# Kernel tuning notes

Hardware: AMD Instinct MI355X
Metric: run time of the kernel (lower is better)

Reference implementation:

```python
import jax, jax.numpy as jnp
import numpy as np

N = 50000      # nodes
E = 800000     # message edges
P = 200000     # prediction edges
C_IN = 64      # in_channels
C_H = 64       # hidden_channels


def setup_inputs() -> dict:
    key = jax.random.key(0)
    ks = jax.random.split(key, 20)
    s = 0.05
    inp = {
        "x": jax.random.normal(ks[0], (N, C_IN), jnp.float32),
        "prediction_edges": jax.random.randint(ks[1], (2, P), 0, N, dtype=jnp.int32),
        "message_edges": jax.random.randint(ks[2], (2, E), 0, N, dtype=jnp.int32),
        "message_edgewt": jax.random.uniform(ks[3], (E,), jnp.float32),
        # conv1 params
        "coef1": jnp.float32(0.5),
        "pool1_w": jax.random.normal(ks[4], (C_IN, C_IN), jnp.float32) * s,
        "pool1_b": jnp.zeros((C_IN,), jnp.float32),
        "fin1_w": jax.random.normal(ks[5], (C_H, 2 * C_IN), jnp.float32) * s,
        "fin1_b": jnp.zeros((C_H,), jnp.float32),
        # conv2 params
        "coef2": jnp.float32(0.5),
        "pool2_w": jax.random.normal(ks[6], (C_H, C_H), jnp.float32) * s,
        "pool2_b": jnp.zeros((C_H,), jnp.float32),
        "fin2_w": jax.random.normal(ks[7], (C_H, 2 * C_H), jnp.float32) * s,
        "fin2_b": jnp.zeros((C_H,), jnp.float32),
        # edge heads
        "ewp_w": jax.random.normal(ks[8], (1, 2 * C_H), jnp.float32) * s,
        "ewp_b": jnp.zeros((1,), jnp.float32),
        "ep_w": jax.random.normal(ks[9], (1, 2 * C_H), jnp.float32) * s,
        "ep_b": jnp.zeros((1,), jnp.float32),
    }
    return inp


def _relu(v):
    return jnp.maximum(v, 0)


def _sage_conv(x, src, dst, ew, coef, pw, pb, fw, fb):
    n = x.shape[0]
    all_src = jnp.concatenate([src, dst])   # [2E]
    all_dst = jnp.concatenate([dst, src])   # [2E]
    neigh = x[all_src]                       # [2E, C] gather
    w2 = jnp.concatenate([ew, ew])           # [2E]
    edge_feat = neigh * (1.0 + coef * w2[:, None])
    pooled = _relu(edge_feat @ pw.T + pb)    # [2E, C]
    # self-loop edges (src == dst) routed to dummy segment n
    seg = jnp.where(all_src != all_dst, all_dst, n)
    agg = jax.ops.segment_max(pooled, seg, num_segments=n + 1)[:n]
    agg = jnp.where(jnp.isfinite(agg), agg, 0.0)  # empty nodes -> 0
    h = jnp.concatenate([x, agg], axis=-1)   # [N, 2C]
    return _relu(h @ fw.T + fb)


def reference(x, prediction_edges, message_edges, message_edgewt,
              coef1, pool1_w, pool1_b, fin1_w, fin1_b,
              coef2, pool2_w, pool2_b, fin2_w, fin2_b,
              ewp_w, ewp_b, ep_w, ep_b):
    src, dst = message_edges[0], message_edges[1]
    h = _sage_conv(x, src, dst, message_edgewt, coef1, pool1_w, pool1_b, fin1_w, fin1_b)
    h = _sage_conv(h, src, dst, message_edgewt, coef2, pool2_w, pool2_b, fin2_w, fin2_b)
    emb = jnp.concatenate([h[prediction_edges[0]], h[prediction_edges[1]]], axis=-1)  # [P, 2C]
    edge_weights = _relu(emb @ ewp_w.T + ewp_b)   # [P, 1]
    edge_predictor = emb @ ep_w.T + ep_b          # [P, 1]
    return edge_weights, edge_predictor
```

## Files before the change

kernel.cpp:

```cpp
#include <hip/hip_runtime.h>


typedef _Float16 h16;
typedef __attribute__((ext_vector_type(4))) _Float16 h16x4;
typedef __attribute__((ext_vector_type(4))) float f32x4;
#define MFMA16(a, b, c) __builtin_amdgcn_mfma_f32_16x16x16f16(a, b, c, 0, 0, 0)

#define NBMAX 1600
#define NFB   128

__global__ void hist_kernel(const int* __restrict__ esrc,
                            const int* __restrict__ edst,
                            int* __restrict__ bucketTotal,
                            int* __restrict__ blockBase, int E, int NB) {
    __shared__ int cnt[NBMAX];
    for (int b = threadIdx.x; b < NB; b += blockDim.x) cnt[b] = 0;
    __syncthreads();
    const int chunk = (E + gridDim.x - 1) / gridDim.x;
    const int start = blockIdx.x * chunk;
    const int end = min(start + chunk, E);
    for (int e = start + (int)threadIdx.x; e < end; e += blockDim.x) {
        const int s = esrc[e];
        const int d = edst[e];
        if (s != d) {
            atomicAdd(&cnt[d >> 5], 1);
            atomicAdd(&cnt[s >> 5], 1);
        }
    }
    __syncthreads();
    for (int b = threadIdx.x; b < NB; b += blockDim.x)
        blockBase[(size_t)blockIdx.x * NB + b] = atomicAdd(&bucketTotal[b], cnt[b]);
}

__global__ void scan_kernel(const int* __restrict__ deg,
                            int* __restrict__ offs, int n) {
    __shared__ int wsum[16];
    __shared__ int s_carry;
    const int tid = threadIdx.x;
    const int lane = tid & 63;
    const int wid = tid >> 6;
    if (tid == 0) s_carry = 0;
    __syncthreads();
    for (int base = 0; base < n; base += 1024) {
        const int i = base + tid;
        const int v = (i < n) ? deg[i] : 0;
        int x = v;
#pragma unroll
        for (int off = 1; off < 64; off <<= 1) {
            int t = __shfl_up(x, off, 64);
            if (lane >= off) x += t;
        }
        if (lane == 63) wsum[wid] = x;
        __syncthreads();
        if (wid == 0) {
            int wv = (lane < 16) ? wsum[lane] : 0;
#pragma unroll
            for (int off = 1; off < 16; off <<= 1) {
                int t = __shfl_up(wv, off, 64);
                if (lane >= off) wv += t;
            }
            if (lane < 16) wsum[lane] = wv;
        }
        __syncthreads();
        const int carry = s_carry;
        const int waveoff = (wid > 0) ? wsum[wid - 1] : 0;
        if (i < n) offs[i] = carry + waveoff + x - v;
        __syncthreads();
        if (tid == 0) s_carry = carry + wsum[15];
        __syncthreads();
    }
}

__global__ void binfill_kernel(const int* __restrict__ esrc,
                               const int* __restrict__ edst,
                               const float* __restrict__ ewt,
                               const int* __restrict__ bucketStart,
                               const int* __restrict__ blockBase,
                               unsigned* __restrict__ entries, int E, int NB) {
    __shared__ int cur[NBMAX];
    for (int b = threadIdx.x; b < NB; b += blockDim.x)
        cur[b] = bucketStart[b] + blockBase[(size_t)blockIdx.x * NB + b];
    __syncthreads();
    const int chunk = (E + gridDim.x - 1) / gridDim.x;
    const int start = blockIdx.x * chunk;
    const int end = min(start + chunk, E);
    for (int e = start + (int)threadIdx.x; e < end; e += blockDim.x) {
        const int s = esrc[e];
        const int d = edst[e];
        if (s != d) {
            const unsigned wq =
                (unsigned)fminf(ewt[e] * 2048.f + 0.5f, 2047.f) << 21;
            const int pd = atomicAdd(&cur[d >> 5], 1);
            entries[pd] = (unsigned)s | ((unsigned)(d & 31) << 16) | wq;
            const int ps = atomicAdd(&cur[s >> 5], 1);
            entries[ps] = (unsigned)d | ((unsigned)(s & 31) << 16) | wq;
        }
    }
}

__global__ void sortbucket_kernel(const int* __restrict__ bucketStart,
                                  const int* __restrict__ bucketTotal,
                                  const unsigned* __restrict__ in,
                                  unsigned* __restrict__ out,
                                  int* __restrict__ nodeBeg, int n, int NB) {
    __shared__ int bin[32];
    __shared__ int cur[32];
    const int bkt = blockIdx.x;
    const int beg = bucketStart[bkt];
    const int cnt = bucketTotal[bkt];
    if (threadIdx.x < 32) bin[threadIdx.x] = 0;
    __syncthreads();
    for (int i = threadIdx.x; i < cnt; i += blockDim.x)
        atomicAdd(&bin[(in[beg + i] >> 16) & 31u], 1);
    __syncthreads();
    if (threadIdx.x == 0) {
        int run = 0;
#pragma unroll
        for (int r = 0; r < 32; ++r) { cur[r] = run; run += bin[r]; }
    }
    __syncthreads();
    if (threadIdx.x < 32) {
        const int node = bkt * 32 + (int)threadIdx.x;
        if (node < n) nodeBeg[node] = beg + cur[threadIdx.x];
    }
    if (bkt == NB - 1 && threadIdx.x == 0) nodeBeg[n] = beg + cnt;
    __syncthreads();
    for (int i = threadIdx.x; i < cnt; i += blockDim.x) {
        const unsigned e = in[beg + i];
        const int pos = beg + atomicAdd(&cur[(e >> 16) & 31u], 1);
        out[pos] = e;
    }
}

template <bool XFP32>
__global__ __launch_bounds__(256, 2)
void mmA_kernel(const void* __restrict__ Xv, const float* __restrict__ W,
                h16* __restrict__ Z, int ntiles) {
    const int lane = threadIdx.x & 63;
    const int c = lane & 15, q = lane >> 4;
    int wave = (int)((blockIdx.x * blockDim.x + threadIdx.x) >> 6);
    const int nwaves = (int)((gridDim.x * blockDim.x) >> 6);
    h16x4 bf[4][4];
#pragma unroll
    for (int ct = 0; ct < 4; ++ct)
#pragma unroll
        for (int ks = 0; ks < 4; ++ks) {
            const float4 w4 = *(const float4*)(W + (ct * 16 + c) * 64 + ks * 16 + q * 4);
            bf[ct][ks] = (h16x4){(h16)w4.x, (h16)w4.y, (h16)w4.z, (h16)w4.w};
        }
    for (int t = wave; t < ntiles; t += nwaves) {
        const int n0 = t * 16;
        h16x4 af[4];
        if constexpr (XFP32) {
            const float* xr = (const float*)Xv + (size_t)(n0 + c) * 64 + q * 4;
#pragma unroll
            for (int ks = 0; ks < 4; ++ks) {
                const float4 v = *(const float4*)(xr + ks * 16);
                af[ks] = (h16x4){(h16)v.x, (h16)v.y, (h16)v.z, (h16)v.w};
            }
        } else {
            const h16* xr = (const h16*)Xv + (size_t)(n0 + c) * 64 + q * 4;
#pragma unroll
            for (int ks = 0; ks < 4; ++ks) af[ks] = *(const h16x4*)(xr + ks * 16);
        }
        f32x4 acc[4];
#pragma unroll
        for (int ct = 0; ct < 4; ++ct) acc[ct] = (f32x4){0.f, 0.f, 0.f, 0.f};
#pragma unroll
        for (int ct = 0; ct < 4; ++ct)
#pragma unroll
            for (int ks = 0; ks < 4; ++ks)
                acc[ct] = MFMA16(af[ks], bf[ct][ks], acc[ct]);
#pragma unroll
        for (int ct = 0; ct < 4; ++ct)
#pragma unroll
            for (int m = 0; m < 4; ++m)
                Z[(size_t)(n0 + q * 4 + m) * 64 + ct * 16 + c] = (h16)acc[ct][m];
    }
}

__global__ void aggregateN_kernel(const int* __restrict__ nodeBeg,
                                  const unsigned* __restrict__ entries,
                                  const h16* __restrict__ Z,
                                  const float* __restrict__ pb,
                                  const float* __restrict__ coefp,
                                  h16* __restrict__ agg, int n) {
    const int lane = threadIdx.x & 63;
    int wave = (int)((blockIdx.x * blockDim.x + threadIdx.x) >> 6);
    const int nwaves = (int)((gridDim.x * blockDim.x) >> 6);
    const float coefq = coefp[0] * (1.f / 2048.f);
    const float pbc = pb[lane];
    for (int d = wave; d < n; d += nwaves) {
        const int du = __builtin_amdgcn_readfirstlane(d);
        const int beg = nodeBeg[du];
        const int end = nodeBeg[du + 1];
        float m0 = 0.f, m1 = 0.f, m2 = 0.f, m3 = 0.f;
        int i = beg;
        for (; i + 4 <= end; i += 4) {
            const unsigned e0 = (unsigned)__builtin_amdgcn_readfirstlane((int)entries[i]);
            const unsigned e1 = (unsigned)__builtin_amdgcn_readfirstlane((int)entries[i + 1]);
            const unsigned e2 = (unsigned)__builtin_amdgcn_readfirstlane((int)entries[i + 2]);
            const unsigned e3 = (unsigned)__builtin_amdgcn_readfirstlane((int)entries[i + 3]);
            const float z0 = (float)Z[(size_t)(e0 & 0xffffu) * 64 + lane];
            const float z1 = (float)Z[(size_t)(e1 & 0xffffu) * 64 + lane];
            const float z2 = (float)Z[(size_t)(e2 & 0xffffu) * 64 + lane];
            const float z3 = (float)Z[(size_t)(e3 & 0xffffu) * 64 + lane];
            m0 = fmaxf(m0, fmaf(fmaf(coefq, (float)(e0 >> 21), 1.f), z0, pbc));
            m1 = fmaxf(m1, fmaf(fmaf(coefq, (float)(e1 >> 21), 1.f), z1, pbc));
            m2 = fmaxf(m2, fmaf(fmaf(coefq, (float)(e2 >> 21), 1.f), z2, pbc));
            m3 = fmaxf(m3, fmaf(fmaf(coefq, (float)(e3 >> 21), 1.f), z3, pbc));
        }
        for (; i < end; ++i) {
            const unsigned e = (unsigned)__builtin_amdgcn_readfirstlane((int)entries[i]);
            const float zv = (float)Z[(size_t)(e & 0xffffu) * 64 + lane];
            m0 = fmaxf(m0, fmaf(fmaf(coefq, (float)(e >> 21), 1.f), zv, pbc));
        }
        agg[(size_t)du * 64 + lane] = (h16)fmaxf(fmaxf(m0, m1), fmaxf(m2, m3));
    }
}

template <bool XFP32>
__global__ __launch_bounds__(256, 2)
void finA_kernel(const void* __restrict__ XA, const h16* __restrict__ XB,
                 const float* __restrict__ W, const float* __restrict__ b,
                 h16* __restrict__ H, int ntiles) {
    const int lane = threadIdx.x & 63;
    const int c = lane & 15, q = lane >> 4;
    int wave = (int)((blockIdx.x * blockDim.x + threadIdx.x) >> 6);
    const int nwaves = (int)((gridDim.x * blockDim.x) >> 6);
    h16x4 bf[4][8];
#pragma unroll
    for (int ct = 0; ct < 4; ++ct)
#pragma unroll
        for (int ks = 0; ks < 8; ++ks) {
            const float4 w4 = *(const float4*)(W + (ct * 16 + c) * 128 + ks * 16 + q * 4);
            bf[ct][ks] = (h16x4){(h16)w4.x, (h16)w4.y, (h16)w4.z, (h16)w4.w};
        }
    float bc[4];
#pragma unroll
    for (int ct = 0; ct < 4; ++ct) bc[ct] = b[ct * 16 + c];
    for (int t = wave; t < ntiles; t += nwaves) {
        const int n0 = t * 16;
        h16x4 af[8];
        if constexpr (XFP32) {
            const float* ra = (const float*)XA + (size_t)(n0 + c) * 64 + q * 4;
#pragma unroll
            for (int ks = 0; ks < 4; ++ks) {
                const float4 v = *(const float4*)(ra + ks * 16);
                af[ks] = (h16x4){(h16)v.x, (h16)v.y, (h16)v.z, (h16)v.w};
            }
        } else {
            const h16* ra = (const h16*)XA + (size_t)(n0 + c) * 64 + q * 4;
#pragma unroll
            for (int ks = 0; ks < 4; ++ks) af[ks] = *(const h16x4*)(ra + ks * 16);
        }
        const h16* rb = XB + (size_t)(n0 + c) * 64 + q * 4;
#pragma unroll
        for (int ks = 0; ks < 4; ++ks) af[4 + ks] = *(const h16x4*)(rb + ks * 16);
        f32x4 acc[4];
#pragma unroll
        for (int ct = 0; ct < 4; ++ct) acc[ct] = (f32x4){bc[ct], bc[ct], bc[ct], bc[ct]};
#pragma unroll
        for (int ct = 0; ct < 4; ++ct)
#pragma unroll
            for (int ks = 0; ks < 8; ++ks)
                acc[ct] = MFMA16(af[ks], bf[ct][ks], acc[ct]);
#pragma unroll
        for (int ct = 0; ct < 4; ++ct)
#pragma unroll
            for (int m = 0; m < 4; ++m)
                H[(size_t)(n0 + q * 4 + m) * 64 + ct * 16 + c] =
                    (h16)fmaxf(acc[ct][m], 0.f);
    }
}

__global__ __launch_bounds__(256, 2)
void fin2A_kernel(const h16* __restrict__ XA, const h16* __restrict__ XB,
                  const float* __restrict__ W, const float* __restrict__ b,
                  const float* __restrict__ ewp_w, const float* __restrict__ ep_w,
                  float4* __restrict__ nodeheads, int ntiles) {
    const int lane = threadIdx.x & 63;
    const int c = lane & 15, q = lane >> 4;
    int wave = (int)((blockIdx.x * blockDim.x + threadIdx.x) >> 6);
    const int nwaves = (int)((gridDim.x * blockDim.x) >> 6);
    h16x4 bf[4][8];
#pragma unroll
    for (int ct = 0; ct < 4; ++ct)
#pragma unroll
        for (int ks = 0; ks < 8; ++ks) {
            const float4 w4 = *(const float4*)(W + (ct * 16 + c) * 128 + ks * 16 + q * 4);
            bf[ct][ks] = (h16x4){(h16)w4.x, (h16)w4.y, (h16)w4.z, (h16)w4.w};
        }
    float bc[4], hw1s[4], hw1d[4], hw2s[4], hw2d[4];
#pragma unroll
    for (int ct = 0; ct < 4; ++ct) {
        bc[ct] = b[ct * 16 + c];
        hw1s[ct] = ewp_w[ct * 16 + c];
        hw1d[ct] = ewp_w[64 + ct * 16 + c];
        hw2s[ct] = ep_w[ct * 16 + c];
        hw2d[ct] = ep_w[64 + ct * 16 + c];
    }
    for (int t = wave; t < ntiles; t += nwaves) {
        const int n0 = t * 16;
        const h16* __restrict__ ra = XA + (size_t)(n0 + c) * 64 + q * 4;
        const h16* __restrict__ rb = XB + (size_t)(n0 + c) * 64 + q * 4;
        h16x4 af[8];
#pragma unroll
        for (int ks = 0; ks < 4; ++ks) {
            af[ks] = *(const h16x4*)(ra + ks * 16);
            af[4 + ks] = *(const h16x4*)(rb + ks * 16);
        }
        f32x4 acc[4];
#pragma unroll
        for (int ct = 0; ct < 4; ++ct) acc[ct] = (f32x4){bc[ct], bc[ct], bc[ct], bc[ct]};
#pragma unroll
        for (int ct = 0; ct < 4; ++ct)
#pragma unroll
            for (int ks = 0; ks < 8; ++ks)
                acc[ct] = MFMA16(af[ks], bf[ct][ks], acc[ct]);
        f32x4 r1 = {0.f, 0.f, 0.f, 0.f}, r2 = r1, r3 = r1, r4 = r1;
#pragma unroll
        for (int ct = 0; ct < 4; ++ct)
#pragma unroll
            for (int m = 0; m < 4; ++m) {
                const float h = fmaxf(acc[ct][m], 0.f);
                r1[m] = fmaf(hw1s[ct], h, r1[m]);
                r2[m] = fmaf(hw1d[ct], h, r2[m]);
                r3[m] = fmaf(hw2s[ct], h, r3[m]);
                r4[m] = fmaf(hw2d[ct], h, r4[m]);
            }
#pragma unroll
        for (int off = 1; off < 16; off <<= 1)
#pragma unroll
            for (int m = 0; m < 4; ++m) {
                r1[m] += __shfl_xor(r1[m], off, 16);
                r2[m] += __shfl_xor(r2[m], off, 16);
                r3[m] += __shfl_xor(r3[m], off, 16);
                r4[m] += __shfl_xor(r4[m], off, 16);
            }
        if (c == 0) {
#pragma unroll
            for (int m = 0; m < 4; ++m)
                nodeheads[n0 + q * 4 + m] =
                    make_float4(r1[m], r2[m], r3[m], r4[m]);
        }
    }
}

__global__ void headsP_kernel(const int* __restrict__ psrc,
                              const int* __restrict__ pdst,
                              const float4* __restrict__ nodeheads,
                              const float* __restrict__ ewp_b,
                              const float* __restrict__ ep_b,
                              float* __restrict__ out, int P) {
    int t = blockIdx.x * blockDim.x + threadIdx.x;
    const int stride = gridDim.x * blockDim.x;
    const float b1 = ewp_b[0], b2 = ep_b[0];
    for (; t < P; t += stride) {
        const float4 qs = nodeheads[psrc[t]];
        const float4 qd = nodeheads[pdst[t]];
        out[t] = fmaxf(qs.x + qd.y + b1, 0.f);
        out[(size_t)P + t] = qs.z + qd.w + b2;
    }
}

extern "C" void kernel_launch(void* const* d_in, const int* in_sizes, int n_in,
                              void* d_out, int out_size, void* d_ws, size_t ws_size,
                              hipStream_t stream) {
    const float* x      = (const float*)d_in[0];
    const int*   pe     = (const int*)d_in[1];
    const int*   me     = (const int*)d_in[2];
    const float* mew    = (const float*)d_in[3];
    const float* coef1  = (const float*)d_in[4];
    const float* p1w    = (const float*)d_in[5];
    const float* p1b    = (const float*)d_in[6];
    const float* f1w    = (const float*)d_in[7];
    const float* f1b    = (const float*)d_in[8];
    const float* coef2  = (const float*)d_in[9];
    const float* p2w    = (const float*)d_in[10];
    const float* p2b    = (const float*)d_in[11];
    const float* f2w    = (const float*)d_in[12];
    const float* f2b    = (const float*)d_in[13];
    const float* ewp_w  = (const float*)d_in[14];
    const float* ewp_b  = (const float*)d_in[15];
    const float* ep_w   = (const float*)d_in[16];
    const float* ep_b   = (const float*)d_in[17];

    const int n = in_sizes[0] / 64;
    const int P = in_sizes[1] / 2;
    const int E = in_sizes[2] / 2;
    const int NB = (n + 31) >> 5;
    const int ntiles = (n + 15) >> 4;

    float4* nodeheads = (float4*)d_ws;
    h16* z16   = (h16*)(nodeheads + n);
    h16* agg16 = z16 + (size_t)n * 64;
    h16* h1    = agg16 + (size_t)n * 64;
    unsigned* entriesA = (unsigned*)(h1 + (size_t)n * 64);
    unsigned* entriesB = entriesA + 2 * (size_t)E;
    int* bucketTotal = (int*)(entriesB + 2 * (size_t)E);
    int* bucketStart = bucketTotal + NBMAX;
    int* nodeBeg     = bucketStart + NBMAX;
    int* blockBase   = nodeBeg + (n + 1);

    const int* esrc = me;
    const int* edst = me + E;
    const int* psrc = pe;
    const int* pdst = pe + P;

    const dim3 blk(256);
    const int mfGrid = (ntiles + 3) / 4;
    const int agGrid = 2048;
    const int hpGrid = (P + 255) / 256;

    hipMemsetAsync(bucketTotal, 0, (size_t)NB * sizeof(int), stream);
    hist_kernel<<<NFB, blk, 0, stream>>>(esrc, edst, bucketTotal, blockBase, E, NB);
    scan_kernel<<<1, 1024, 0, stream>>>(bucketTotal, bucketStart, NB);
    binfill_kernel<<<NFB, blk, 0, stream>>>(esrc, edst, mew, bucketStart,
                                            blockBase, entriesA, E, NB);
    sortbucket_kernel<<<NB, blk, 0, stream>>>(bucketStart, bucketTotal,
                                              entriesA, entriesB, nodeBeg, n, NB);

    mmA_kernel<true><<<mfGrid, blk, 0, stream>>>(x, p1w, z16, ntiles);
    aggregateN_kernel<<<agGrid, blk, 0, stream>>>(nodeBeg, entriesB, z16,
                                                  p1b, coef1, agg16, n);
    finA_kernel<true><<<mfGrid, blk, 0, stream>>>(x, agg16, f1w, f1b, h1, ntiles);

    mmA_kernel<false><<<mfGrid, blk, 0, stream>>>(h1, p2w, z16, ntiles);
    aggregateN_kernel<<<agGrid, blk, 0, stream>>>(nodeBeg, entriesB, z16,
                                                  p2b, coef2, agg16, n);
    fin2A_kernel<<<mfGrid, blk, 0, stream>>>(h1, agg16, f2w, f2b,
                                             ewp_w, ep_w, nodeheads, ntiles);

    headsP_kernel<<<hpGrid, blk, 0, stream>>>(psrc, pdst, nodeheads,
                                              ewp_b, ep_b, (float*)d_out, P);
}
```

Baseline: 201.3 us.

## Fuse bucket scan into binfill, fuse fin1 with pool2 matmul, pair-node aggregation

The separate single-block scan kernel is removed: every binfill block now recomputes the bucket prefix sum in LDS, and block 0 writes bucketStart for the later sort. The layer-1 final linear kernel now also applies the pool2 matmul through an LDS transpose, so the separate mmA launch and its re-read of h1 go away. The aggregation kernel handles two destination nodes per wave with interleaved edge loops, giving more independent gathers in flight per wave. The cost is redundant scan work in every binfill block and higher register and LDS use in the fused kernels.

New measurement: 191.0 us. 1.05x faster.

```diff
diff --git a/kernel.cpp b/kernel.cpp
--- a/kernel.cpp
+++ b/kernel.cpp
@@ -32,67 +32,54 @@
         blockBase[(size_t)blockIdx.x * NB + b] = atomicAdd(&bucketTotal[b], cnt[b]);
 }
 
-__global__ void scan_kernel(const int* __restrict__ deg,
-                            int* __restrict__ offs, int n) {
-    __shared__ int wsum[16];
-    __shared__ int s_carry;
+__global__ void binfill_kernel(const int* __restrict__ esrc,
+                               const int* __restrict__ edst,
+                               const float* __restrict__ ewt,
+                               const int* __restrict__ bucketTotal,
+                               int* __restrict__ bucketStart,
+                               const int* __restrict__ blockBase,
+                               unsigned* __restrict__ entries, int E, int NB) {
+    __shared__ int sv[NBMAX];
+    __shared__ int wls[4];
     const int tid = threadIdx.x;
     const int lane = tid & 63;
     const int wid = tid >> 6;
-    if (tid == 0) s_carry = 0;
-    __syncthreads();
-    for (int base = 0; base < n; base += 1024) {
-        const int i = base + tid;
-        const int v = (i < n) ? deg[i] : 0;
-        int x = v;
-#pragma unroll
-        for (int off = 1; off < 64; off <<= 1) {
-            int t = __shfl_up(x, off, 64);
-            if (lane >= off) x += t;
-        }
-        if (lane == 63) wsum[wid] = x;
-        __syncthreads();
-        if (wid == 0) {
-            int wv = (lane < 16) ? wsum[lane] : 0;
-#pragma unroll
-            for (int off = 1; off < 16; off <<= 1) {
-                int t = __shfl_up(wv, off, 64);
-                if (lane >= off) wv += t;
-            }
-            if (lane < 16) wsum[lane] = wv;
-        }
-        __syncthreads();
-        const int carry = s_carry;
-        const int waveoff = (wid > 0) ? wsum[wid - 1] : 0;
-        if (i < n) offs[i] = carry + waveoff + x - v;
-        __syncthreads();
-        if (tid == 0) s_carry = carry + wsum[15];
-        __syncthreads();
-    }
-}
-
-__global__ void binfill_kernel(const int* __restrict__ esrc,
-                               const int* __restrict__ edst,
-                               const float* __restrict__ ewt,
-                               const int* __restrict__ bucketStart,
-                               const int* __restrict__ blockBase,
-                               unsigned* __restrict__ entries, int E, int NB) {
-    __shared__ int cur[NBMAX];
-    for (int b = threadIdx.x; b < NB; b += blockDim.x)
-        cur[b] = bucketStart[b] + blockBase[(size_t)blockIdx.x * NB + b];
+    for (int b = tid; b < NB; b += blockDim.x) sv[b] = bucketTotal[b];
+    __syncthreads();
+    const int CH = (NB + 255) / 256;
+    const int lo = tid * CH, hi = min(lo + CH, NB);
+    int sum = 0;
+    for (int i = lo; i < hi; ++i) sum += sv[i];
+    int x = sum;
+#pragma unroll
+    for (int off = 1; off < 64; off <<= 1) {
+        int t = __shfl_up(x, off, 64);
+        if (lane >= off) x += t;
+    }
+    if (lane == 63) wls[wid] = x;
+    __syncthreads();
+    int wof = 0;
+    for (int w = 0; w < wid; ++w) wof += wls[w];
+    int run = wof + x - sum;
+    for (int i = lo; i < hi; ++i) { const int v = sv[i]; sv[i] = run; run += v; }
+    __syncthreads();
+    if (blockIdx.x == 0)
+        for (int b = tid; b < NB; b += blockDim.x) bucketStart[b] = sv[b];
+    for (int b = tid; b < NB; b += blockDim.x)
+        sv[b] += blockBase[(size_t)blockIdx.x * NB + b];
     __syncthreads();
     const int chunk = (E + gridDim.x - 1) / gridDim.x;
     const int start = blockIdx.x * chunk;
     const int end = min(start + chunk, E);
-    for (int e = start + (int)threadIdx.x; e < end; e += blockDim.x) {
+    for (int e = start + (int)tid; e < end; e += blockDim.x) {
         const int s = esrc[e];
         const int d = edst[e];
         if (s != d) {
             const unsigned wq =
                 (unsigned)fminf(ewt[e] * 2048.f + 0.5f, 2047.f) << 21;
-            const int pd = atomicAdd(&cur[d >> 5], 1);
+            const int pd = atomicAdd(&sv[d >> 5], 1);
             entries[pd] = (unsigned)s | ((unsigned)(d & 31) << 16) | wq;
-            const int ps = atomicAdd(&cur[s >> 5], 1);
+            const int ps = atomicAdd(&sv[s >> 5], 1);
             entries[ps] = (unsigned)d | ((unsigned)(s & 31) << 16) | wq;
         }
     }
@@ -179,7 +166,13 @@
     }
 }
 
-__global__ void aggregateN_kernel(const int* __restrict__ nodeBeg,
+#define EDGE_STEP(eV, mV)                                                      \
+    {                                                                          \
+        const float zv = (float)Z[(size_t)((eV) & 0xffffu) * 64 + lane];       \
+        mV = fmaxf(mV, fmaf(fmaf(coefq, (float)((eV) >> 21), 1.f), zv, pbc));  \
+    }
+
+__global__ void aggregateP_kernel(const int* __restrict__ nodeBeg,
                                   const unsigned* __restrict__ entries,
                                   const h16* __restrict__ Z,
                                   const float* __restrict__ pb,
@@ -190,69 +183,96 @@
     const int nwaves = (int)((gridDim.x * blockDim.x) >> 6);
     const float coefq = coefp[0] * (1.f / 2048.f);
     const float pbc = pb[lane];
-    for (int d = wave; d < n; d += nwaves) {
-        const int du = __builtin_amdgcn_readfirstlane(d);
-        const int beg = nodeBeg[du];
-        const int end = nodeBeg[du + 1];
-        float m0 = 0.f, m1 = 0.f, m2 = 0.f, m3 = 0.f;
-        int i = beg;
-        for (; i + 4 <= end; i += 4) {
-            const unsigned e0 = (unsigned)__builtin_amdgcn_readfirstlane((int)entries[i]);
-            const unsigned e1 = (unsigned)__builtin_amdgcn_readfirstlane((int)entries[i + 1]);
-            const unsigned e2 = (unsigned)__builtin_amdgcn_readfirstlane((int)entries[i + 2]);
-            const unsigned e3 = (unsigned)__builtin_amdgcn_readfirstlane((int)entries[i + 3]);
-            const float z0 = (float)Z[(size_t)(e0 & 0xffffu) * 64 + lane];
-            const float z1 = (float)Z[(size_t)(e1 & 0xffffu) * 64 + lane];
-            const float z2 = (float)Z[(size_t)(e2 & 0xffffu) * 64 + lane];
-            const float z3 = (float)Z[(size_t)(e3 & 0xffffu) * 64 + lane];
-            m0 = fmaxf(m0, fmaf(fmaf(coefq, (float)(e0 >> 21), 1.f), z0, pbc));
-            m1 = fmaxf(m1, fmaf(fmaf(coefq, (float)(e1 >> 21), 1.f), z1, pbc));
-            m2 = fmaxf(m2, fmaf(fmaf(coefq, (float)(e2 >> 21), 1.f), z2, pbc));
-            m3 = fmaxf(m3, fmaf(fmaf(coefq, (float)(e3 >> 21), 1.f), z3, pbc));
-        }
-        for (; i < end; ++i) {
-            const unsigned e = (unsigned)__builtin_amdgcn_readfirstlane((int)entries[i]);
-            const float zv = (float)Z[(size_t)(e & 0xffffu) * 64 + lane];
-            m0 = fmaxf(m0, fmaf(fmaf(coefq, (float)(e >> 21), 1.f), zv, pbc));
-        }
-        agg[(size_t)du * 64 + lane] = (h16)fmaxf(fmaxf(m0, m1), fmaxf(m2, m3));
-    }
-}
-
-template <bool XFP32>
+    const int npairs = (n + 1) >> 1;
+    for (int p = wave; p < npairs; p += nwaves) {
+        const int dA = __builtin_amdgcn_readfirstlane(2 * p);
+        const int dB = dA + 1;
+        const int begA = nodeBeg[dA];
+        const int endA = nodeBeg[dA + 1];
+        int iB = endA, endB = endA;
+        if (dB < n) endB = nodeBeg[dB + 1];
+        float mA0 = 0.f, mA1 = 0.f, mA2 = 0.f, mA3 = 0.f;
+        float mB0 = 0.f, mB1 = 0.f, mB2 = 0.f, mB3 = 0.f;
+        int iA = begA;
+        while (iA + 4 <= endA && iB + 4 <= endB) {
+            const unsigned a0 = (unsigned)__builtin_amdgcn_readfirstlane((int)entries[iA]);
+            const unsigned a1 = (unsigned)__builtin_amdgcn_readfirstlane((int)entries[iA + 1]);
+            const unsigned a2 = (unsigned)__builtin_amdgcn_readfirstlane((int)entries[iA + 2]);
+            const unsigned a3 = (unsigned)__builtin_amdgcn_readfirstlane((int)entries[iA + 3]);
+            const unsigned b0 = (unsigned)__builtin_amdgcn_readfirstlane((int)entries[iB]);
+            const unsigned b1 = (unsigned)__builtin_amdgcn_readfirstlane((int)entries[iB + 1]);
+            const unsigned b2 = (unsigned)__builtin_amdgcn_readfirstlane((int)entries[iB + 2]);
+            const unsigned b3 = (unsigned)__builtin_amdgcn_readfirstlane((int)entries[iB + 3]);
+            EDGE_STEP(a0, mA0) EDGE_STEP(a1, mA1) EDGE_STEP(a2, mA2) EDGE_STEP(a3, mA3)
+            EDGE_STEP(b0, mB0) EDGE_STEP(b1, mB1) EDGE_STEP(b2, mB2) EDGE_STEP(b3, mB3)
+            iA += 4; iB += 4;
+        }
+        for (; iA + 4 <= endA; iA += 4) {
+            const unsigned a0 = (unsigned)__builtin_amdgcn_readfirstlane((int)entries[iA]);
+            const unsigned a1 = (unsigned)__builtin_amdgcn_readfirstlane((int)entries[iA + 1]);
+            const unsigned a2 = (unsigned)__builtin_amdgcn_readfirstlane((int)entries[iA + 2]);
+            const unsigned a3 = (unsigned)__builtin_amdgcn_readfirstlane((int)entries[iA + 3]);
+            EDGE_STEP(a0, mA0) EDGE_STEP(a1, mA1) EDGE_STEP(a2, mA2) EDGE_STEP(a3, mA3)
+        }
+        for (; iB + 4 <= endB; iB += 4) {
+            const unsigned b0 = (unsigned)__builtin_amdgcn_readfirstlane((int)entries[iB]);
+            const unsigned b1 = (unsigned)__builtin_amdgcn_readfirstlane((int)entries[iB + 1]);
+            const unsigned b2 = (unsigned)__builtin_amdgcn_readfirstlane((int)entries[iB + 2]);
+            const unsigned b3 = (unsigned)__builtin_amdgcn_readfirstlane((int)entries[iB + 3]);
+            EDGE_STEP(b0, mB0) EDGE_STEP(b1, mB1) EDGE_STEP(b2, mB2) EDGE_STEP(b3, mB3)
+        }
+        for (; iA < endA; ++iA) {
+            const unsigned a0 = (unsigned)__builtin_amdgcn_readfirstlane((int)entries[iA]);
+            EDGE_STEP(a0, mA0)
+        }
+        for (; iB < endB; ++iB) {
+            const unsigned b0 = (unsigned)__builtin_amdgcn_readfirstlane((int)entries[iB]);
+            EDGE_STEP(b0, mB0)
+        }
+        agg[(size_t)dA * 64 + lane] = (h16)fmaxf(fmaxf(mA0, mA1), fmaxf(mA2, mA3));
+        if (dB < n)
+            agg[(size_t)dB * 64 + lane] = (h16)fmaxf(fmaxf(mB0, mB1), fmaxf(mB2, mB3));
+    }
+}
+
 __global__ __launch_bounds__(256, 2)
-void finA_kernel(const void* __restrict__ XA, const h16* __restrict__ XB,
-                 const float* __restrict__ W, const float* __restrict__ b,
-                 h16* __restrict__ H, int ntiles) {
+void finAmm_kernel(const float* __restrict__ XA, const h16* __restrict__ XB,
+                   const float* __restrict__ W, const float* __restrict__ b,
+                   const float* __restrict__ W2,
+                   h16* __restrict__ H, h16* __restrict__ Z2, int ntiles) {
+    __shared__ h16 ldsT[4][16 * 68];
     const int lane = threadIdx.x & 63;
+    const int wid = threadIdx.x >> 6;
     const int c = lane & 15, q = lane >> 4;
     int wave = (int)((blockIdx.x * blockDim.x + threadIdx.x) >> 6);
     const int nwaves = (int)((gridDim.x * blockDim.x) >> 6);
-    h16x4 bf[4][8];
-#pragma unroll
-    for (int ct = 0; ct < 4; ++ct)
+    h16x4 bf[4][8], bf2[4][4];
+#pragma unroll
+    for (int ct = 0; ct < 4; ++ct) {
 #pragma unroll
         for (int ks = 0; ks < 8; ++ks) {
             const float4 w4 = *(const float4*)(W + (ct * 16 + c) * 128 + ks * 16 + q * 4);
             bf[ct][ks] = (h16x4){(h16)w4.x, (h16)w4.y, (h16)w4.z, (h16)w4.w};
         }
+#pragma unroll
+        for (int ks = 0; ks < 4; ++ks) {
+            const float4 w4 = *(const float4*)(W2 + (ct * 16 + c) * 64 + ks * 16 + q * 4);
+            bf2[ct][ks] = (h16x4){(h16)w4.x, (h16)w4.y, (h16)w4.z, (h16)w4.w};
+        }
+    }
     float bc[4];
 #pragma unroll
     for (int ct = 0; ct < 4; ++ct) bc[ct] = b[ct * 16 + c];
     for (int t = wave; t < ntiles; t += nwaves) {
         const int n0 = t * 16;
         h16x4 af[8];
-        if constexpr (XFP32) {
-            const float* ra = (const float*)XA + (size_t)(n0 + c) * 64 + q * 4;
+        {
+            const float* ra = XA + (size_t)(n0 + c) * 64 + q * 4;
 #pragma unroll
             for (int ks = 0; ks < 4; ++ks) {
                 const float4 v = *(const float4*)(ra + ks * 16);
                 af[ks] = (h16x4){(h16)v.x, (h16)v.y, (h16)v.z, (h16)v.w};
             }
-        } else {
-            const h16* ra = (const h16*)XA + (size_t)(n0 + c) * 64 + q * 4;
-#pragma unroll
-            for (int ks = 0; ks < 4; ++ks) af[ks] = *(const h16x4*)(ra + ks * 16);
         }
         const h16* rb = XB + (size_t)(n0 + c) * 64 + q * 4;
 #pragma unroll
@@ -268,9 +288,28 @@
 #pragma unroll
         for (int ct = 0; ct < 4; ++ct)
 #pragma unroll
+            for (int m = 0; m < 4; ++m) {
+                const h16 hv = (h16)fmaxf(acc[ct][m], 0.f);
+                H[(size_t)(n0 + q * 4 + m) * 64 + ct * 16 + c] = hv;
+                ldsT[wid][(q * 4 + m) * 68 + ct * 16 + c] = hv;
+            }
+        h16x4 af2[4];
+#pragma unroll
+        for (int ks = 0; ks < 4; ++ks)
+            af2[ks] = *(const h16x4*)&ldsT[wid][c * 68 + ks * 16 + q * 4];
+        f32x4 acc2[4];
+#pragma unroll
+        for (int ct = 0; ct < 4; ++ct) acc2[ct] = (f32x4){0.f, 0.f, 0.f, 0.f};
+#pragma unroll
+        for (int ct = 0; ct < 4; ++ct)
+#pragma unroll
+            for (int ks = 0; ks < 4; ++ks)
+                acc2[ct] = MFMA16(af2[ks], bf2[ct][ks], acc2[ct]);
+#pragma unroll
+        for (int ct = 0; ct < 4; ++ct)
+#pragma unroll
             for (int m = 0; m < 4; ++m)
-                H[(size_t)(n0 + q * 4 + m) * 64 + ct * 16 + c] =
-                    (h16)fmaxf(acc[ct][m], 0.f);
+                Z2[(size_t)(n0 + q * 4 + m) * 64 + ct * 16 + c] = (h16)acc2[ct][m];
     }
 }
 
@@ -415,19 +454,18 @@
 
     hipMemsetAsync(bucketTotal, 0, (size_t)NB * sizeof(int), stream);
     hist_kernel<<<NFB, blk, 0, stream>>>(esrc, edst, bucketTotal, blockBase, E, NB);
-    scan_kernel<<<1, 1024, 0, stream>>>(bucketTotal, bucketStart, NB);
-    binfill_kernel<<<NFB, blk, 0, stream>>>(esrc, edst, mew, bucketStart,
-                                            blockBase, entriesA, E, NB);
+    binfill_kernel<<<NFB, blk, 0, stream>>>(esrc, edst, mew, bucketTotal,
+                                            bucketStart, blockBase, entriesA, E, NB);
     sortbucket_kernel<<<NB, blk, 0, stream>>>(bucketStart, bucketTotal,
                                               entriesA, entriesB, nodeBeg, n, NB);
 
     mmA_kernel<true><<<mfGrid, blk, 0, stream>>>(x, p1w, z16, ntiles);
-    aggregateN_kernel<<<agGrid, blk, 0, stream>>>(nodeBeg, entriesB, z16,
+    aggregateP_kernel<<<agGrid, blk, 0, stream>>>(nodeBeg, entriesB, z16,
                                                   p1b, coef1, agg16, n);
-    finA_kernel<true><<<mfGrid, blk, 0, stream>>>(x, agg16, f1w, f1b, h1, ntiles);
-
-    mmA_kernel<false><<<mfGrid, blk, 0, stream>>>(h1, p2w, z16, ntiles);
-    aggregateN_kernel<<<agGrid, blk, 0, stream>>>(nodeBeg, entriesB, z16,
+    finAmm_kernel<<<mfGrid, blk, 0, stream>>>(x, agg16, f1w, f1b, p2w,
+                                              h1, z16, ntiles);
+
+    aggregateP_kernel<<<agGrid, blk, 0, stream>>>(nodeBeg, entriesB, z16,
                                                   p2b, coef2, agg16, n);
     fin2A_kernel<<<mfGrid, blk, 0, stream>>>(h1, agg16, f2w, f2b,
                                              ewp_w, ep_w, nodeheads, ntiles);
```
